# Kernel optimization log

Hardware: AMD Instinct MI355X
Metric: run time of the kernel (lower is better)

## Reference

```python
import jax, jax.numpy as jnp
import numpy as np

NB, H, C, HID, EMB = 4, 12, 1024, 768, 512
E, M, L, SPAN = 22, 4, 16, 32
TD, INTER = 20, 256
NN = E + E * M + L
NREL, NLAYERS = 3, 4

def _build_adj():
    # static relational adjacency: r0 entity<->its mentions, r1 mention<->co-entity mention, r2 mention<->link
    A = np.zeros((NREL, NN, NN), np.float32)
    for e in range(E):
        for m in range(M):
            mi = E + e * M + m
            A[0, e, mi] = A[0, mi, e] = 1.0
            for m2 in range(M):
                if m2 != m:
                    A[1, mi, E + e * M + m2] = 1.0
            li = E + E * M + ((e * M + m) % L)
            A[2, mi, li] = A[2, li, mi] = 1.0
    A = A / (A.sum(-1, keepdims=True) + 1e-5)
    return jnp.asarray(A)

_ADJ = _build_adj()
_TYPES = np.concatenate([np.zeros(E, np.int32), np.ones(E * M, np.int32), np.full(L, 2, np.int32)])

def _forward(sequence_output, attention, W_trans, b_trans, type_embed,
             rgcn_Wrel0, rgcn_Wself0, rgcn_Wrel, rgcn_Wself,
             fs_w1, fs_b1, fs_g1, fs_be1, fs_w2, fs_b2, fs_g2, fs_be2,
             fc_w1, fc_b1, fc_g1, fc_be1, fc_w2, fc_b2, fc_g2, fc_be2,
             cr_w1, cr_b1, cr_w2, cr_b2, cr_w3, cr_b3,
             mention_idx, link_start):
    n = sequence_output.shape[0]
    b = jnp.arange(n)[:, None, None]
    seq = sequence_output @ W_trans + b_trans            # [n,C,EMB] extractor_trans
    attq = attention.transpose(0, 2, 1, 3)               # [n,C,H,C] query-major
    # --- make_graph: mention / entity nodes (gather + logsumexp pooling) ---
    m_rep = seq[b, mention_idx]                          # [n,E,M,EMB]
    m_att = attq[b, mention_idx]                         # [n,E,M,H,C]
    e_rep = jax.nn.logsumexp(m_rep, axis=2)              # [n,E,EMB]
    e_att = m_att.mean(axis=2)                           # [n,E,H,C]
    # --- link nodes: attention-weighted span pooling ---
    idx = link_start[:, :, None] + jnp.arange(SPAN)      # [n,L,SPAN]
    span = seq[b, idx]                                   # [n,L,SPAN,EMB]
    att_rows = attq[b, idx]                              # [n,L,SPAN,H,C]
    col_idx = jnp.broadcast_to(idx[:, :, None, None, :], (n, L, SPAN, H, SPAN))
    block = jnp.take_along_axis(att_rows, col_idx, axis=4).mean(axis=3)  # [n,L,SPAN,SPAN]
    link_rep = jnp.einsum('nlst,nltd->nld', block, span) / SPAN          # [n,L,EMB]
    # --- node matrix + type embedding ---
    nodes = jnp.concatenate([e_rep, m_rep.reshape(n, E * M, EMB), link_rep], axis=1)
    tfeat = jnp.broadcast_to(type_embed[_TYPES][None], (n, NN, TD))
    h = jnp.concatenate([nodes, tfeat], axis=-1)         # [n,NN,EMB+TD]
    # --- RGCN ---
    def rgcn_layer(hh, Wrel, Wself):
        msg = jnp.einsum('rij,njd,rdo->nio', _ADJ, hh, Wrel)
        return jax.nn.relu(msg + hh @ Wself)
    h = rgcn_layer(h, rgcn_Wrel0, rgcn_Wself0)
    for l in range(NLAYERS - 1):
        h = rgcn_layer(h, rgcn_Wrel[l], rgcn_Wself[l])
    # --- relation_map: structure + attention-weighted context ---
    entity_stru = h[:, :E]                               # [n,E,EMB]
    ea = e_att.mean(axis=2)                              # [n,E,C]
    ea = ea / (ea.sum(-1, keepdims=True) + 1e-5)
    e_ctx = jnp.einsum('nec,ncd->ned', ea, seq)          # [n,E,EMB]
    ec = entity_stru + e_ctx
    fmap = (ec[:, :, None, :] * ec[:, None, :, :]).transpose(0, 3, 1, 2)  # [n,EMB,E,E]
    # --- SE fusion (fusion_s / fusion_c, BN in eval form) ---
    conv1x1 = lambda x, w, bb: jnp.einsum('nchw,oc->nohw', x, w) + bb[None, :, None, None]
    bn = lambda x, g, be: x * g[None, :, None, None] + be[None, :, None, None]
    s = bn(conv1x1(jax.nn.relu(bn(conv1x1(fmap, fs_w1, fs_b1), fs_g1, fs_be1)), fs_w2, fs_b2), fs_g2, fs_be2)
    pooled = fmap.mean(axis=(2, 3), keepdims=True)
    cb = bn(conv1x1(jax.nn.relu(bn(conv1x1(pooled, fc_w1, fc_b1), fc_g1, fc_be1)), fc_w2, fc_b2), fc_g2, fc_be2)
    fused = fmap * jax.nn.sigmoid(s + cb)
    # --- conv_reason 5x5 blocks ---
    dn = ('NCHW', 'OIHW', 'NCHW')
    conv = lambda x, w, bb: jax.lax.conv_general_dilated(x, w, (1, 1), 'SAME', dimension_numbers=dn) + bb[None, :, None, None]
    r = jax.nn.relu(conv(fused, cr_w1, cr_b1))
    r = jax.nn.relu(conv(r, cr_w2, cr_b2))
    return jax.nn.relu(conv(r, cr_w3, cr_b3))            # [n,EMB,E,E]

def setup_inputs():
    key = jax.random.key(0)
    ks = jax.random.split(key, 24)
    p = lambda k, sh: jax.random.normal(k, sh, jnp.float32) * 0.02
    z = lambda sh: jnp.zeros(sh, jnp.float32)
    o = lambda sh: jnp.ones(sh, jnp.float32)
    return {
        'sequence_output': jax.random.normal(ks[0], (NB, C, HID), jnp.float32),
        'attention': jax.random.uniform(ks[1], (NB, H, C, C), jnp.float32),
        'W_trans': p(ks[2], (HID, EMB)), 'b_trans': z((EMB,)),
        'type_embed': p(ks[3], (3, TD)),
        'rgcn_Wrel0': p(ks[4], (NREL, EMB + TD, EMB)), 'rgcn_Wself0': p(ks[5], (EMB + TD, EMB)),
        'rgcn_Wrel': p(ks[6], (NLAYERS - 1, NREL, EMB, EMB)), 'rgcn_Wself': p(ks[7], (NLAYERS - 1, EMB, EMB)),
        'fs_w1': p(ks[8], (INTER, EMB)), 'fs_b1': z((INTER,)), 'fs_g1': o((INTER,)), 'fs_be1': z((INTER,)),
        'fs_w2': p(ks[9], (EMB, INTER)), 'fs_b2': z((EMB,)), 'fs_g2': o((EMB,)), 'fs_be2': z((EMB,)),
        'fc_w1': p(ks[10], (INTER, EMB)), 'fc_b1': z((INTER,)), 'fc_g1': o((INTER,)), 'fc_be1': z((INTER,)),
        'fc_w2': p(ks[11], (EMB, INTER)), 'fc_b2': z((EMB,)), 'fc_g2': o((EMB,)), 'fc_be2': z((EMB,)),
        'cr_w1': p(ks[12], (INTER, EMB, 5, 5)), 'cr_b1': z((INTER,)),
        'cr_w2': p(ks[13], (INTER, INTER, 5, 5)), 'cr_b2': z((INTER,)),
        'cr_w3': p(ks[14], (EMB, INTER, 5, 5)), 'cr_b3': z((EMB,)),
        'mention_idx': jax.random.randint(ks[15], (NB, E, M), 0, C),
        'link_start': jnp.sort(jax.random.randint(ks[16], (NB, L), 0, C - SPAN), axis=-1),
    }

def reference(sequence_output, attention, W_trans, b_trans, type_embed,
              rgcn_Wrel0, rgcn_Wself0, rgcn_Wrel, rgcn_Wself,
              fs_w1, fs_b1, fs_g1, fs_be1, fs_w2, fs_b2, fs_g2, fs_be2,
              fc_w1, fc_b1, fc_g1, fc_be1, fc_w2, fc_b2, fc_g2, fc_be2,
              cr_w1, cr_b1, cr_w2, cr_b2, cr_w3, cr_b3,
              mention_idx, link_start):
    return _forward(sequence_output, attention, W_trans, b_trans, type_embed,
                    rgcn_Wrel0, rgcn_Wself0, rgcn_Wrel, rgcn_Wself,
                    fs_w1, fs_b1, fs_g1, fs_be1, fs_w2, fs_b2, fs_g2, fs_be2,
                    fc_w1, fc_b1, fc_g1, fc_be1, fc_w2, fc_b2, fc_g2, fc_be2,
                    cr_w1, cr_b1, cr_w2, cr_b2, cr_w3, cr_b3,
                    mention_idx, link_start)
```

## Files before the change

kernel.cpp:

```cpp
#include <hip/hip_runtime.h>
#include <hip/hip_bf16.h>
#include <stdint.h>

typedef long long ll;
typedef float f32x4 __attribute__((ext_vector_type(4)));
typedef __bf16 bf16x8 __attribute__((ext_vector_type(8)));
typedef __bf16 bf16x4 __attribute__((ext_vector_type(4)));

__global__ void k_prep(const float* __restrict__ cr_w1, const float* __restrict__ cr_w2,
                       const float* __restrict__ cr_w3, __bf16* __restrict__ Wt1,
                       __bf16* __restrict__ Wt2, __bf16* __restrict__ Wt3,
                       const float* __restrict__ W_trans, __bf16* __restrict__ wth,
                       __bf16* __restrict__ wtl,
                       const float* __restrict__ Wrel0, const float* __restrict__ Wself0,
                       __bf16* __restrict__ wc0h, __bf16* __restrict__ wc0l,
                       const float* __restrict__ Wrel, const float* __restrict__ Wself,
                       __bf16* __restrict__ wc13h, __bf16* __restrict__ wc13l,
                       uint4* __restrict__ XintZ)
{
  __shared__ float t[32][33];
  int b = blockIdx.x; int tid = threadIdx.x;
  if (b < 1024){
    const float* w; __bf16* dst; int C, o;
    if (b < 256){ w=cr_w1; dst=Wt1; C=512; o=b; }
    else if (b < 512){ w=cr_w2; dst=Wt2; C=256; o=b-256; }
    else { w=cr_w3; dst=Wt3; C=256; o=b-512; }
    for (int c=tid; c<C; c+=256){
      const float* src = w + ((size_t)o*C + c)*25;
      float v[25];
      #pragma unroll
      for (int q=0;q<25;q++) v[q] = src[q];
      #pragma unroll
      for (int q=0;q<25;q++) dst[((size_t)o*25 + q)*C + c] = (__bf16)v[q];
    }
  } else if (b < 2560){
    ll idx = (ll)(b-1024)*256 + tid;
    int r = (int)(idx % 768); int c = (int)(idx / 768);
    float x = W_trans[(ll)r*512 + c];
    __bf16 h = (__bf16)x;
    wth[idx] = h; wtl[idx] = (__bf16)(x - (float)h);
  } else if (b < 6720){
    int Din, Kpad, KD, bx, by;
    const float* wr; const float* ws2; __bf16* hb; __bf16* lb;
    if (b < 3648){
      int b2 = b-2560; bx = b2 % 68; by = b2/68; Din=532; Kpad=2176; KD=544;
      wr = Wrel0; ws2 = Wself0; hb = wc0h; lb = wc0l;
    } else {
      int b3 = b-3648; int l = b3/1024; int r2 = b3%1024; bx = r2%64; by = r2/64;
      Din=512; Kpad=2048; KD=512;
      wr = Wrel + (ll)l*3*512*512; ws2 = Wself + (ll)l*512*512;
      hb = wc13h + (ll)l*512*2048; lb = wc13l + (ll)l*512*2048;
    }
    int k0 = bx*32, o0 = by*32;
    int tx = tid&31, ty = tid>>5;
    for (int j=ty; j<32; j+=8){
      int k = k0 + j; float v = 0.f;
      int r = k / KD, d = k - r*KD;
      if (d < Din && r < 4)
        v = (r<3) ? wr[((ll)(r*Din+d))*512 + o0+tx] : ws2[(ll)d*512 + o0+tx];
      t[j][tx] = v;
    }
    __syncthreads();
    for (int j=ty; j<32; j+=8){
      float x = t[tx][j];
      __bf16 h = (__bf16)x;
      hb[(ll)(o0+j)*Kpad + k0+tx] = h;
      lb[(ll)(o0+j)*Kpad + k0+tx] = (__bf16)(x - (float)h);
    }
  } else {
    ll idx = (ll)(b-6720)*256 + tid;
    if (idx < 475136){
      uint4 z; z.x=0u; z.y=0u; z.z=0u; z.w=0u;
      XintZ[idx] = z;
    }
  }
}

template<int SPLIT, int MODE, int BN, int FMAPB>
__global__ __launch_bounds__(512) void gemm_mfma(
    const float* __restrict__ A,
    const __bf16* __restrict__ Bhi, const __bf16* __restrict__ Blo,
    float* __restrict__ Cf, __bf16* __restrict__ Cb,
    int M, int N, int K, ll sA, ll sB, ll sC,
    const float* __restrict__ biasN, const float* __restrict__ biasM,
    const float* __restrict__ gM, const float* __restrict__ beM,
    const float* __restrict__ Hf, const float* __restrict__ Ec,
// ... 158 lines not shown
    float* C = Cf + sC*b;
    #pragma unroll
    for (int mf=0; mf<2; ++mf){
      int gmb = m0 + wave_m0 + mf*16 + lg*4;
      #pragma unroll
      for (int nf=0; nf<NF; ++nf){
        int gn = n0 + wave_n0 + nf*16 + l15;
        if (gn >= N) continue;
        float bn_ = (MODE==0 && biasN) ? biasN[gn] : 0.f;
        f32x4 a = acc[mf][nf];
        #pragma unroll
        for (int r=0;r<4;r++){
          int gm = gmb + r;
          if (gm < M){
            float v = a[r] + bn_;
            if (MODE==1) v = fmaxf(v, 0.f);
            C[(ll)gm*N + gn] = v;
          }
        }
      }
    }
  } else if (MODE==2){
    __bf16* C = Cb + sC*b;
    #pragma unroll
    for (int mf=0; mf<2; ++mf){
      int gmb = m0 + wave_m0 + mf*16 + lg*4;
      float b0=biasM[gmb], b1=biasM[gmb+1], b2=biasM[gmb+2], b3=biasM[gmb+3];
      float g0=gM[gmb], g1=gM[gmb+1], g2=gM[gmb+2], g3=gM[gmb+3];
      float e0=beM[gmb], e1=beM[gmb+1], e2=beM[gmb+2], e3=beM[gmb+3];
      #pragma unroll
      for (int nf=0; nf<NF; ++nf){
        int gn = n0 + wave_n0 + nf*16 + l15;
        if (gn >= N) continue;
        f32x4 a = acc[mf][nf];
        union { bf16x4 v; uint2 u; } pk;
        pk.v[0] = (__bf16)fmaxf((a[0]+b0)*g0+e0, 0.f);
        pk.v[1] = (__bf16)fmaxf((a[1]+b1)*g1+e1, 0.f);
        pk.v[2] = (__bf16)fmaxf((a[2]+b2)*g2+e2, 0.f);
        pk.v[3] = (__bf16)fmaxf((a[3]+b3)*g3+e3, 0.f);
        *reinterpret_cast<uint2*>(C + (ll)gn*M + gmb) = pk.u;
      }
    }
  } else {
    __bf16* C = Cb + sC*b;
    const float* cb = CBV + (ll)b*512;
    #pragma unroll
    for (int mf=0; mf<2; ++mf){
      int gmb = m0 + wave_m0 + mf*16 + lg*4;
      float b0=biasM[gmb], b1=biasM[gmb+1], b2=biasM[gmb+2], b3=biasM[gmb+3];
      float g0=gM[gmb], g1=gM[gmb+1], g2=gM[gmb+2], g3=gM[gmb+3];
      float e0=beM[gmb], e1=beM[gmb+1], e2=beM[gmb+2], e3=beM[gmb+3];
      float c0=cb[gmb], c1=cb[gmb+1], c2=cb[gmb+2], c3=cb[gmb+3];
      #pragma unroll
      for (int nf=0; nf<NF; ++nf){
        int gn = n0 + wave_n0 + nf*16 + l15;
        if (gn >= N) continue;
        f32x4 a = acc[mf][nf];
        int pi = gn/22, pj = gn%22;
        float4 hi4 = *reinterpret_cast<const float4*>(Hf + ((ll)b*126+pi)*512 + gmb);
        float4 ei4 = *reinterpret_cast<const float4*>(Ec + ((ll)b*22 +pi)*512 + gmb);
        float4 hj4 = *reinterpret_cast<const float4*>(Hf + ((ll)b*126+pj)*512 + gmb);
        float4 ej4 = *reinterpret_cast<const float4*>(Ec + ((ll)b*22 +pj)*512 + gmb);
        float fm0 = (hi4.x+ei4.x)*(hj4.x+ej4.x);
        float fm1 = (hi4.y+ei4.y)*(hj4.y+ej4.y);
        float fm2 = (hi4.z+ei4.z)*(hj4.z+ej4.z);
        float fm3 = (hi4.w+ei4.w)*(hj4.w+ej4.w);
        float s0 = (a[0]+b0)*g0+e0 + c0;
        float s1 = (a[1]+b1)*g1+e1 + c1;
        float s2 = (a[2]+b2)*g2+e2 + c2;
        float s3 = (a[3]+b3)*g3+e3 + c3;
        union { bf16x4 v; uint2 u; } pk;
        pk.v[0] = (__bf16)(fm0 / (1.f + expf(-s0)));
        pk.v[1] = (__bf16)(fm1 / (1.f + expf(-s1)));
        pk.v[2] = (__bf16)(fm2 / (1.f + expf(-s2)));
        pk.v[3] = (__bf16)(fm3 / (1.f + expf(-s3)));
        int py = gn/22, px = gn%22;
        int e = (py+2)*32 + px + 2;
        *reinterpret_cast<uint2*>(C + (ll)e*512 + gmb) = pk.u;
      }
    }
  }
}

template<int CIN, int OCHT, int OT, bool FINAL>
__global__ __launch_bounds__(256) void conv5_mfma(
    const __bf16* __restrict__ Xg, const __bf16* __restrict__ Wt,
    const float* __restrict__ bias, __bf16* __restrict__ Xout,
    float* __restrict__ outF)
{
  constexpr int OF = OT/32;
  constexpr int WCH = OT*4;
  __shared__ bf16x8 Xs8[272*32/8];
  __shared__ bf16x8 Ws8[5*OT*32/8];
  char* xs = (char*)Xs8;
  char* wsm = (char*)Ws8;

  const int tid = threadIdx.x;
  const int l = tid & 63;
  const int l15 = l & 15, lg = l >> 4, lg16 = (l>>4)*16;
  const int w = tid >> 6;
  const int wave_o0 = (w>>1)*(OT/2);
  const int wave_p0 = (w&1)*64;
  const int b = blockIdx.z;
  const int p0 = blockIdx.x*128;
  const int o0 = blockIdx.y*OT;

  int baseA[OF];
  #pragma unroll
  for (int of=0; of<OF; ++of){
    int orow = wave_o0 + of*16 + l15;
    baseA[of] = orow*64 + (lg16 ^ (((orow>>1)&3)<<4));
  }
  int pl[4];
  #pragma unroll
  for (int pf=0; pf<4; ++pf) pl[pf] = wave_p0 + pf*16 + l15;

  f32x4 acc[OF][4] = {};

  const int NCB = CIN/32;
  for (int cblk=0; cblk<NCB; ++cblk){
    __syncthreads();
    #pragma unroll
    for (int i=0;i<5;i++){
      int idx = tid + i*256;
      if (idx < 1088){
        int e = idx>>2, c8 = idx&3;
        const __bf16* g = Xg + ((size_t)(b*928 + p0 + e))*CIN + cblk*32 + c8*8;
        bf16x8 v = *reinterpret_cast<const bf16x8*>(g);
        int byte = e*64 + ((c8*16) ^ (((e>>1)&3)<<4));
        *reinterpret_cast<bf16x8*>(xs + byte) = v;
      }
    }
    for (int g5=0; g5<5; ++g5){
      if (g5>0) __syncthreads();
      #pragma unroll
      for (int i=0;i<(5*WCH+255)/256;i++){
        int idx = tid + i*256;
        if (idx < 5*WCH){
          int tapL = idx/WCH, r = idx%WCH;
          int o = r>>2, c8 = r&3;
          const __bf16* g = Wt + ((size_t)(o0+o)*25 + (g5*5+tapL))*CIN + cblk*32 + c8*8;
          bf16x8 v = *reinterpret_cast<const bf16x8*>(g);
          int byte = tapL*(OT*64) + o*64 + ((c8*16) ^ (((o>>1)&3)<<4));
          *reinterpret_cast<bf16x8*>(wsm + byte) = v;
        }
      }
      __syncthreads();
      #pragma unroll
      for (int tapL=0; tapL<5; ++tapL){
        bf16x8 a[OF];
        #pragma unroll
        for (int of=0; of<OF; ++of)
          a[of] = *reinterpret_cast<const bf16x8*>(wsm + tapL*(OT*64) + baseA[of]);
        int koff = g5*32 + tapL;
        #pragma unroll
        for (int pf=0; pf<4; ++pf){
          int e = pl[pf] + koff;
          bf16x8 bv = *reinterpret_cast<const bf16x8*>(xs + e*64 + (lg16 ^ (((e>>1)&3)<<4)));
          #pragma unroll
          for (int of=0; of<OF; ++of)
            acc[of][pf] = __builtin_amdgcn_mfma_f32_16x16x32_bf16(a[of], bv, acc[of][pf], 0,0,0);
        }
      }
    }
  }

  #pragma unroll
  for (int of=0; of<OF; ++of){
    int og = o0 + wave_o0 + of*16 + lg*4;
    float b0 = bias[og], b1 = bias[og+1], b2 = bias[og+2], b3 = bias[og+3];
    #pragma unroll
    for (int pf=0; pf<4; ++pf){
      int p = p0 + pl[pf];
      int py = p>>5, px = p&31;
      if (py>=22 || px>=22) continue;
      f32x4 a = acc[of][pf];
      float v0 = fmaxf(a[0]+b0, 0.f), v1 = fmaxf(a[1]+b1, 0.f);
      float v2 = fmaxf(a[2]+b2, 0.f), v3 = fmaxf(a[3]+b3, 0.f);
      if (FINAL){
        size_t base = ((size_t)b*OCHT + og)*484 + py*22 + px;
        outF[base] = v0; outF[base+484] = v1; outF[base+968] = v2; outF[base+1452] = v3;
      } else {
        union { bf16x4 v; uint2 u; } pk;
        pk.v[0] = (__bf16)v0; pk.v[1] = (__bf16)v1; pk.v[2] = (__bf16)v2; pk.v[3] = (__bf16)v3;
        int e = p + 66;
        *reinterpret_cast<uint2*>(Xout + ((size_t)(b*928 + e))*OCHT + og) = pk.u;
      }
    }
  }
}

__global__ void k_gather(const float* __restrict__ seq, const float* __restrict__ att,
                         const int* __restrict__ midx, const int* __restrict__ ls_,
                         const float* __restrict__ te, float* __restrict__ h0,
                         float* __restrict__ ea, __bf16* __restrict__ sqTh,
                         __bf16* __restrict__ sqTl)
{
  __shared__ float part[32][8];
  __shared__ float wv[32];
  __shared__ float vals[1024];
  __shared__ float red[256];
  __shared__ float tt2[32][33];
  int b = blockIdx.x; int t = threadIdx.x;
  if (b < 88){
    int n = b/22, e = b%22;
    int rows[4];
    #pragma unroll
    for (int m=0;m<4;m++) rows[m] = midx[(n*22+e)*4+m];
    for (int d=t; d<512; d+=256){
      float v[4]; float mx = -1e30f;
      #pragma unroll
      for (int m=0;m<4;m++){
        v[m] = seq[((ll)n*1024+rows[m])*512 + d];
        h0[((ll)n*126+22+e*4+m)*532 + d] = v[m];
        mx = fmaxf(mx, v[m]);
      }
      float s = 0.f;
      #pragma unroll
      for (int m=0;m<4;m++) s += expf(v[m]-mx);
      h0[((ll)n*126+e)*532 + d] = mx + logf(s);
    }
  } else if (b < 152){
    int bb = b-88;
    int n = bb/16, l = bb%16;
    int ls = ls_[n*16+l];
    int tt = t>>3, lane = t&7;
    float acc = 0.f;
    for (int i=lane; i<384; i+=8){
      int h = i>>5, s = i&31;
      acc += att[((ll)(n*12+h)*1024 + ls+s)*1024 + (ls+tt)];
    }
    part[tt][lane] = acc; __syncthreads();
    if (lane==0){
      float s2=0.f;
      #pragma unroll
      for (int q=0;q<8;q++) s2 += part[tt][q];
      wv[tt] = s2*(1.f/12.f);
    }
    __syncthreads();
    for (int d=t; d<512; d+=256){
      float a2 = 0.f;
      for (int tk=0;tk<32;tk++) a2 += wv[tk]*seq[((ll)n*1024+ls+tk)*512 + d];
      h0[((ll)n*126+110+l)*532 + d] = a2*(1.f/32.f);
    }
  } else if (b < 192){
    int idx = (b-152)*256 + t;
    if (idx < 4*126*20){
      int q = idx%20; int i = (idx/20)%126; int n = idx/(20*126);
      int ty = (i<22)?0:((i<110)?1:2);
      h0[((ll)n*126+i)*532 + 512 + q] = te[ty*20+q];
    }
  } else if (b < 280){
    int bb = b-192;
    int n = bb/22, e = bb%22;
    int rows[4];
    #pragma unroll
    for (int m=0;m<4;m++) rows[m] = midx[(n*22+e)*4+m];
    float local = 0.f;
    for (int c=t; c<1024; c+=256){
      float acc = 0.f;
      #pragma unroll
      for (int m=0;m<4;m++){
        const float* base = att + ((ll)n*12*1024 + rows[m])*1024 + c;
        #pragma unroll
        for (int h=0;h<12;h++) acc += base[(ll)h*1048576];
      }
      acc *= (1.f/48.f);
      vals[c] = acc; local += acc;
    }
    red[t] = local; __syncthreads();
    for (int s=128;s>0;s>>=1){ if (t<s) red[t]+=red[t+s]; __syncthreads(); }
    float denom = red[0] + 1e-5f;
    for (int c=t; c<1024; c+=256) ea[((ll)bb)*1024 + c] = vals[c]/denom;
  } else {
    int b2 = b-280;
    int n = b2>>9; int rem = b2&511;
    int r0 = (rem&31)*32, c0 = (rem>>5)*32;
    int tx = t&31, ty = t>>5;
    for (int j=ty; j<32; j+=8)
      tt2[j][tx] = seq[((ll)n*1024 + r0+j)*512 + c0+tx];
    __syncthreads();
    for (int j=ty; j<32; j+=8){
      float x = tt2[tx][j];
      __bf16 h = (__bf16)x;
      ll o = ((ll)n*512 + c0+j)*1024 + r0+tx;
      sqTh[o] = h; sqTl[o] = (__bf16)(x - (float)h);
    }
  }
}

__global__ void k_buildX_s(const float* __restrict__ h, float* __restrict__ X,
                           int Din, int KD){
  int n = blockIdx.x/126, i = blockIdx.x%126;
  const float* hb = h + (ll)n*126*Din;
  ll rowoff = (ll)(n*126+i)*4*KD;
  const float inv1 = 1.f/(1.f+1e-5f), inv3 = 1.f/(3.f+1e-5f), inv4 = 1.f/(4.f+1e-5f);
  for (int d=threadIdx.x; d<KD; d+=256){
    float m0v=0.f, m1v=0.f, m2v=0.f, hh=0.f;
    if (d < Din){
      if (i < 22){
        int base = 22 + i*4;
        float s = hb[(ll)(base+0)*Din+d] + hb[(ll)(base+1)*Din+d]
                + hb[(ll)(base+2)*Din+d] + hb[(ll)(base+3)*Din+d];
        m0v = s * inv4;
      } else if (i < 110){
        int em = i-22, e = em>>2, base = 22+(e<<2);
        m0v = hb[(ll)e*Din+d] * inv1;
        float s1 = 0.f;
        #pragma unroll
        for (int m2=0;m2<4;m2++) if (base+m2 != i) s1 += hb[(ll)(base+m2)*Din+d];
        m1v = s1 * inv3;
        m2v = hb[(ll)(110+(em&15))*Din+d] * inv1;
      } else {
        int li0 = i-110;
        int cnt = (li0<8)?6:5;
        float s = 0.f;
        for (int t2=0;t2<cnt;t2++) s += hb[(ll)(22+li0+16*t2)*Din+d];
        m2v = s / ((float)cnt + 1e-5f);
      }
      hh = hb[(ll)i*Din+d];
    }
    X[rowoff + 0*KD + d] = m0v;
    X[rowoff + 1*KD + d] = m1v;
    X[rowoff + 2*KD + d] = m2v;
    X[rowoff + 3*KD + d] = hh;
  }
}

__global__ void k_poolcb(const float* __restrict__ hfin, const float* __restrict__ ectx,
                         const float* __restrict__ w1, const float* __restrict__ b1,
                         const float* __restrict__ g1, const float* __restrict__ be1,
                         const float* __restrict__ w2, const float* __restrict__ b2,
                         const float* __restrict__ g2, const float* __restrict__ be2,
                         float* __restrict__ cb){
  __shared__ float ps[512], t1[256];
  int n = blockIdx.x; int t = threadIdx.x;
  for (int c=t; c<512; c+=256){
    float s = 0.f;
    for (int i=0;i<22;i++)
      s += hfin[((ll)n*126+i)*512 + c] + ectx[((ll)n*22+i)*512 + c];
    ps[c] = s*s*(1.f/484.f);
  }
  __syncthreads();
  {
    float acc = 0.f;
    for (int c=0;c<512;c++) acc += w1[t*512+c]*ps[c];
    float v = g1[t]*(acc+b1[t]) + be1[t];
    t1[t] = fmaxf(v, 0.f);
  }
  __syncthreads();
  for (int o=t; o<512; o+=256){
    float acc = 0.f;
    for (int c=0;c<256;c++) acc += w2[o*256+c]*t1[c];
    cb[n*512+o] = g2[o]*(acc+b2[o]) + be2[o];
  }
}

extern "C" void kernel_launch(void* const* d_in, const int* in_sizes, int n_in,
                              void* d_out, int out_size, void* d_ws, size_t ws_size,
                              hipStream_t stream)
{
  (void)in_sizes; (void)n_in; (void)out_size; (void)ws_size;
  const float* seqout   = (const float*)d_in[0];
  const float* att      = (const float*)d_in[1];
  const float* W_trans  = (const float*)d_in[2];
  const float* b_trans  = (const float*)d_in[3];
  const float* type_emb = (const float*)d_in[4];
  const float* Wrel0    = (const float*)d_in[5];
  const float* Wself0   = (const float*)d_in[6];
  const float* Wrel     = (const float*)d_in[7];
  const float* Wself    = (const float*)d_in[8];
  const float* fs_w1    = (const float*)d_in[9];
  const float* fs_b1    = (const float*)d_in[10];
  const float* fs_g1    = (const float*)d_in[11];
  const float* fs_be1   = (const float*)d_in[12];
  const float* fs_w2    = (const float*)d_in[13];
  const float* fs_b2    = (const float*)d_in[14];
  const float* fs_g2    = (const float*)d_in[15];
  const float* fs_be2   = (const float*)d_in[16];
  const float* fc_w1    = (const float*)d_in[17];
  const float* fc_b1    = (const float*)d_in[18];
  const float* fc_g1    = (const float*)d_in[19];
  const float* fc_be1   = (const float*)d_in[20];
  const float* fc_w2    = (const float*)d_in[21];
  const float* fc_b2    = (const float*)d_in[22];
  const float* fc_g2    = (const float*)d_in[23];
  const float* fc_be2   = (const float*)d_in[24];
  const float* cr_w1    = (const float*)d_in[25];
  const float* cr_b1    = (const float*)d_in[26];
  const float* cr_w2    = (const float*)d_in[27];
  const float* cr_b2    = (const float*)d_in[28];
  const float* cr_w3    = (const float*)d_in[29];
  const float* cr_b3    = (const float*)d_in[30];
  const int*   midx     = (const int*)d_in[31];
  const int*   lstart   = (const int*)d_in[32];
  float* out            = (float*)d_out;

  char* wsb = (char*)d_ws;
  size_t off = 0;
  auto allocB = [&](size_t nbytes)->char*{ char* p = wsb + off; off += (nbytes + 63) & ~(size_t)63; return p; };
  float* seq   = (float*)allocB((size_t)4096*512*4);
  float* h0    = (float*)allocB((size_t)504*532*4);
  float* ea    = (float*)allocB((size_t)88*1024*4);
  float* ectx  = (float*)allocB((size_t)88*512*4);
  float* X     = (float*)allocB((size_t)504*2176*4);
  float* hA    = (float*)allocB((size_t)504*512*4);
  float* hB    = (float*)allocB((size_t)504*512*4);
  float* cbv   = (float*)allocB(2048*4);
  __bf16* wth  = (__bf16*)allocB((size_t)512*768*2);
  __bf16* wtl  = (__bf16*)allocB((size_t)512*768*2);
  __bf16* sqTh = (__bf16*)allocB((size_t)4*512*1024*2);
  __bf16* sqTl = (__bf16*)allocB((size_t)4*512*1024*2);
  __bf16* wc0h = (__bf16*)allocB((size_t)512*2176*2);
  __bf16* wc0l = (__bf16*)allocB((size_t)512*2176*2);
  __bf16* wc13h= (__bf16*)allocB((size_t)3*512*2048*2);
  __bf16* wc13l= (__bf16*)allocB((size_t)3*512*2048*2);
  __bf16* s1bT = (__bf16*)allocB((size_t)4*484*256*2);
  __bf16* Xint1 = (__bf16*)allocB((size_t)4*928*512*2);
  __bf16* Xint2 = (__bf16*)allocB((size_t)4*928*256*2);
  __bf16* Xint3 = (__bf16*)allocB((size_t)4*928*256*2);
  __bf16* Wt1   = (__bf16*)allocB((size_t)256*25*512*2);
  __bf16* Wt2   = (__bf16*)allocB((size_t)256*25*256*2);
  __bf16* Wt3   = (__bf16*)allocB((size_t)512*25*256*2);

  k_prep<<<8576,256,0,stream>>>(cr_w1, cr_w2, cr_w3, Wt1, Wt2, Wt3,
                                W_trans, wth, wtl,
                                Wrel0, Wself0, wc0h, wc0l,
                                Wrel, Wself, wc13h, wc13l,
                                reinterpret_cast<uint4*>(Xint1));

  gemm_mfma<1,0,128,0><<<dim3(4,64,1),512,0,stream>>>(seqout, wth, wtl, seq, nullptr,
      4096,512,768, 0,0,0, b_trans,nullptr,nullptr,nullptr, nullptr,nullptr,nullptr);
  k_gather<<<2328,256,0,stream>>>(seq, att, midx, lstart, type_emb, h0, ea, sqTh, sqTl);
  gemm_mfma<1,0,64,0><<<dim3(8,1,4),512,0,stream>>>(ea, sqTh, sqTl, ectx, nullptr,
      22,512,1024, (ll)22*1024, (ll)512*1024, (ll)22*512,
      nullptr,nullptr,nullptr,nullptr, nullptr,nullptr,nullptr);
  k_buildX_s<<<504,256,0,stream>>>(h0, X, 532, 544);
  gemm_mfma<1,1,32,0><<<dim3(16,8,1),512,0,stream>>>(X, wc0h, wc0l, hA, nullptr,
      504,512,2176, 0,0,0, nullptr,nullptr,nullptr,nullptr, nullptr,nullptr,nullptr);
  float* hcur = hA; float* hnxt = hB;
  for (int l=0;l<3;l++){
    k_buildX_s<<<504,256,0,stream>>>(hcur, X, 512, 512);
    gemm_mfma<1,1,32,0><<<dim3(16,8,1),512,0,stream>>>(X,
        wc13h + (ll)l*512*2048, wc13l + (ll)l*512*2048, hnxt, nullptr,
        504,512,2048, 0,0,0, nullptr,nullptr,nullptr,nullptr, nullptr,nullptr,nullptr);
    float* t = hcur; hcur = hnxt; hnxt = t;
  }
  k_poolcb<<<4,256,0,stream>>>(hcur, ectx, fc_w1, fc_b1, fc_g1, fc_be1,
                               fc_w2, fc_b2, fc_g2, fc_be2, cbv);
  gemm_mfma<0,2,64,1><<<dim3(8,4,4),512,0,stream>>>(fs_w1, nullptr, nullptr, nullptr, s1bT,
      256,484,512, 0, 0, (ll)484*256,
      nullptr, fs_b1, fs_g1, fs_be1, hcur, ectx, nullptr);
  gemm_mfma<0,4,64,0><<<dim3(8,8,4),512,0,stream>>>(fs_w2, s1bT, nullptr, nullptr, Xint1,
      512,484,256, 0, (ll)484*256, (ll)928*512,
      nullptr, fs_b2, fs_g2, fs_be2, hcur, ectx, cbv);
  conv5_mfma<512,256,32,false><<<dim3(6,8,4),256,0,stream>>>(Xint1, Wt1, cr_b1, Xint2, nullptr);
  conv5_mfma<256,256,32,false><<<dim3(6,8,4),256,0,stream>>>(Xint2, Wt2, cr_b2, Xint3, nullptr);
  conv5_mfma<256,512,32,true ><<<dim3(6,16,4),256,0,stream>>>(Xint3, Wt3, cr_b3, nullptr, out);
}
```

Measured before the change: 539.9 us.

## Fuse RGCN layers into one cooperative kernel and widen conv output tiles

```diff
diff --git a/kernel.cpp b/kernel.cpp
--- a/kernel.cpp
+++ b/kernel.cpp
@@ -1,7 +1,9 @@
 #include <hip/hip_runtime.h>
 #include <hip/hip_bf16.h>
+#include <hip/hip_cooperative_groups.h>
 #include <stdint.h>
 
+namespace cg = cooperative_groups;
 typedef long long ll;
 typedef float f32x4 __attribute__((ext_vector_type(4)));
 typedef __bf16 bf16x8 __attribute__((ext_vector_type(8)));
@@ -326,220 +328,15 @@
   }
 }
 
-template<int CIN, int OCHT, int OT, bool FINAL>
-__global__ __launch_bounds__(256) void conv5_mfma(
-    const __bf16* __restrict__ Xg, const __bf16* __restrict__ Wt,
-    const float* __restrict__ bias, __bf16* __restrict__ Xout,
-    float* __restrict__ outF)
-{
-  constexpr int OF = OT/32;
-  constexpr int WCH = OT*4;
-  __shared__ bf16x8 Xs8[272*32/8];
-  __shared__ bf16x8 Ws8[5*OT*32/8];
-  char* xs = (char*)Xs8;
-  char* wsm = (char*)Ws8;
-
-  const int tid = threadIdx.x;
-  const int l = tid & 63;
-  const int l15 = l & 15, lg = l >> 4, lg16 = (l>>4)*16;
-  const int w = tid >> 6;
-  const int wave_o0 = (w>>1)*(OT/2);
-  const int wave_p0 = (w&1)*64;
-  const int b = blockIdx.z;
-  const int p0 = blockIdx.x*128;
-  const int o0 = blockIdx.y*OT;
-
-  int baseA[OF];
-  #pragma unroll
-  for (int of=0; of<OF; ++of){
-    int orow = wave_o0 + of*16 + l15;
-    baseA[of] = orow*64 + (lg16 ^ (((orow>>1)&3)<<4));
-  }
-  int pl[4];
-  #pragma unroll
-  for (int pf=0; pf<4; ++pf) pl[pf] = wave_p0 + pf*16 + l15;
-
-  f32x4 acc[OF][4] = {};
-
-  const int NCB = CIN/32;
-  for (int cblk=0; cblk<NCB; ++cblk){
-    __syncthreads();
-    #pragma unroll
-    for (int i=0;i<5;i++){
-      int idx = tid + i*256;
-      if (idx < 1088){
-        int e = idx>>2, c8 = idx&3;
-        const __bf16* g = Xg + ((size_t)(b*928 + p0 + e))*CIN + cblk*32 + c8*8;
-        bf16x8 v = *reinterpret_cast<const bf16x8*>(g);
-        int byte = e*64 + ((c8*16) ^ (((e>>1)&3)<<4));
-        *reinterpret_cast<bf16x8*>(xs + byte) = v;
-      }
-    }
-    for (int g5=0; g5<5; ++g5){
-      if (g5>0) __syncthreads();
-      #pragma unroll
-      for (int i=0;i<(5*WCH+255)/256;i++){
-        int idx = tid + i*256;
-        if (idx < 5*WCH){
-          int tapL = idx/WCH, r = idx%WCH;
-          int o = r>>2, c8 = r&3;
-          const __bf16* g = Wt + ((size_t)(o0+o)*25 + (g5*5+tapL))*CIN + cblk*32 + c8*8;
-          bf16x8 v = *reinterpret_cast<const bf16x8*>(g);
-          int byte = tapL*(OT*64) + o*64 + ((c8*16) ^ (((o>>1)&3)<<4));
-          *reinterpret_cast<bf16x8*>(wsm + byte) = v;
-        }
-      }
-      __syncthreads();
-      #pragma unroll
-      for (int tapL=0; tapL<5; ++tapL){
-        bf16x8 a[OF];
-        #pragma unroll
-        for (int of=0; of<OF; ++of)
-          a[of] = *reinterpret_cast<const bf16x8*>(wsm + tapL*(OT*64) + baseA[of]);
-        int koff = g5*32 + tapL;
-        #pragma unroll
-        for (int pf=0; pf<4; ++pf){
-          int e = pl[pf] + koff;
-          bf16x8 bv = *reinterpret_cast<const bf16x8*>(xs + e*64 + (lg16 ^ (((e>>1)&3)<<4)));
-          #pragma unroll
-          for (int of=0; of<OF; ++of)
-            acc[of][pf] = __builtin_amdgcn_mfma_f32_16x16x32_bf16(a[of], bv, acc[of][pf], 0,0,0);
-        }
-      }
-    }
-  }
-
-  #pragma unroll
-  for (int of=0; of<OF; ++of){
-    int og = o0 + wave_o0 + of*16 + lg*4;
-    float b0 = bias[og], b1 = bias[og+1], b2 = bias[og+2], b3 = bias[og+3];
-    #pragma unroll
-    for (int pf=0; pf<4; ++pf){
-      int p = p0 + pl[pf];
-      int py = p>>5, px = p&31;
-      if (py>=22 || px>=22) continue;
-      f32x4 a = acc[of][pf];
-      float v0 = fmaxf(a[0]+b0, 0.f), v1 = fmaxf(a[1]+b1, 0.f);
-      float v2 = fmaxf(a[2]+b2, 0.f), v3 = fmaxf(a[3]+b3, 0.f);
-      if (FINAL){
-        size_t base = ((size_t)b*OCHT + og)*484 + py*22 + px;
-        outF[base] = v0; outF[base+484] = v1; outF[base+968] = v2; outF[base+1452] = v3;
-      } else {
-        union { bf16x4 v; uint2 u; } pk;
-        pk.v[0] = (__bf16)v0; pk.v[1] = (__bf16)v1; pk.v[2] = (__bf16)v2; pk.v[3] = (__bf16)v3;
-        int e = p + 66;
-        *reinterpret_cast<uint2*>(Xout + ((size_t)(b*928 + e))*OCHT + og) = pk.u;
-      }
-    }
-  }
-}
-
-__global__ void k_gather(const float* __restrict__ seq, const float* __restrict__ att,
-                         const int* __restrict__ midx, const int* __restrict__ ls_,
-                         const float* __restrict__ te, float* __restrict__ h0,
-                         float* __restrict__ ea, __bf16* __restrict__ sqTh,
-                         __bf16* __restrict__ sqTl)
-{
-  __shared__ float part[32][8];
-  __shared__ float wv[32];
-  __shared__ float vals[1024];
-  __shared__ float red[256];
-  __shared__ float tt2[32][33];
-  int b = blockIdx.x; int t = threadIdx.x;
-  if (b < 88){
-    int n = b/22, e = b%22;
-    int rows[4];
-    #pragma unroll
-    for (int m=0;m<4;m++) rows[m] = midx[(n*22+e)*4+m];
-    for (int d=t; d<512; d+=256){
-      float v[4]; float mx = -1e30f;
-      #pragma unroll
-      for (int m=0;m<4;m++){
-        v[m] = seq[((ll)n*1024+rows[m])*512 + d];
-        h0[((ll)n*126+22+e*4+m)*532 + d] = v[m];
-        mx = fmaxf(mx, v[m]);
-      }
-      float s = 0.f;
-      #pragma unroll
-      for (int m=0;m<4;m++) s += expf(v[m]-mx);
-      h0[((ll)n*126+e)*532 + d] = mx + logf(s);
-    }
-  } else if (b < 152){
-    int bb = b-88;
-    int n = bb/16, l = bb%16;
-    int ls = ls_[n*16+l];
-    int tt = t>>3, lane = t&7;
-    float acc = 0.f;
-    for (int i=lane; i<384; i+=8){
-      int h = i>>5, s = i&31;
-      acc += att[((ll)(n*12+h)*1024 + ls+s)*1024 + (ls+tt)];
-    }
-    part[tt][lane] = acc; __syncthreads();
-    if (lane==0){
-      float s2=0.f;
-      #pragma unroll
-      for (int q=0;q<8;q++) s2 += part[tt][q];
-      wv[tt] = s2*(1.f/12.f);
-    }
-    __syncthreads();
-    for (int d=t; d<512; d+=256){
-      float a2 = 0.f;
-      for (int tk=0;tk<32;tk++) a2 += wv[tk]*seq[((ll)n*1024+ls+tk)*512 + d];
-      h0[((ll)n*126+110+l)*532 + d] = a2*(1.f/32.f);
-    }
-  } else if (b < 192){
-    int idx = (b-152)*256 + t;
-    if (idx < 4*126*20){
-      int q = idx%20; int i = (idx/20)%126; int n = idx/(20*126);
-      int ty = (i<22)?0:((i<110)?1:2);
-      h0[((ll)n*126+i)*532 + 512 + q] = te[ty*20+q];
-    }
-  } else if (b < 280){
-    int bb = b-192;
-    int n = bb/22, e = bb%22;
-    int rows[4];
-    #pragma unroll
-    for (int m=0;m<4;m++) rows[m] = midx[(n*22+e)*4+m];
-    float local = 0.f;
-    for (int c=t; c<1024; c+=256){
-      float acc = 0.f;
-      #pragma unroll
-      for (int m=0;m<4;m++){
-        const float* base = att + ((ll)n*12*1024 + rows[m])*1024 + c;
-        #pragma unroll
-        for (int h=0;h<12;h++) acc += base[(ll)h*1048576];
-      }
-      acc *= (1.f/48.f);
-      vals[c] = acc; local += acc;
-    }
-    red[t] = local; __syncthreads();
-    for (int s=128;s>0;s>>=1){ if (t<s) red[t]+=red[t+s]; __syncthreads(); }
-    float denom = red[0] + 1e-5f;
-    for (int c=t; c<1024; c+=256) ea[((ll)bb)*1024 + c] = vals[c]/denom;
-  } else {
-    int b2 = b-280;
-    int n = b2>>9; int rem = b2&511;
-    int r0 = (rem&31)*32, c0 = (rem>>5)*32;
-    int tx = t&31, ty = t>>5;
-    for (int j=ty; j<32; j+=8)
-      tt2[j][tx] = seq[((ll)n*1024 + r0+j)*512 + c0+tx];
-    __syncthreads();
-    for (int j=ty; j<32; j+=8){
-      float x = tt2[tx][j];
-      __bf16 h = (__bf16)x;
-      ll o = ((ll)n*512 + c0+j)*1024 + r0+tx;
-      sqTh[o] = h; sqTl[o] = (__bf16)(x - (float)h);
-    }
-  }
-}
-
-__global__ void k_buildX_s(const float* __restrict__ h, float* __restrict__ X,
-                           int Din, int KD){
-  int n = blockIdx.x/126, i = blockIdx.x%126;
-  const float* hb = h + (ll)n*126*Din;
-  ll rowoff = (ll)(n*126+i)*4*KD;
+__device__ __forceinline__ void buildX_phase(const float* __restrict__ h,
+                                             float* __restrict__ X, int Din, int KD){
   const float inv1 = 1.f/(1.f+1e-5f), inv3 = 1.f/(3.f+1e-5f), inv4 = 1.f/(4.f+1e-5f);
-  for (int d=threadIdx.x; d<KD; d+=256){
+  int total = 504*KD;
+  for (int idx = blockIdx.x*512 + threadIdx.x; idx < total; idx += 128*512){
+    int row = idx / KD;
+    int d = idx - row*KD;
+    int n = row/126, i = row - n*126;
+    const float* hb = h + (ll)n*126*Din;
     float m0v=0.f, m1v=0.f, m2v=0.f, hh=0.f;
     if (d < Din){
       if (i < 22){
@@ -564,10 +361,364 @@
       }
       hh = hb[(ll)i*Din+d];
     }
+    ll rowoff = (ll)row*4*KD;
     X[rowoff + 0*KD + d] = m0v;
     X[rowoff + 1*KD + d] = m1v;
     X[rowoff + 2*KD + d] = m2v;
     X[rowoff + 3*KD + d] = hh;
+  }
+}
+
+__device__ __forceinline__ void rgcn_gemm_phase(
+    const float* __restrict__ A, const __bf16* __restrict__ Bhi,
+    const __bf16* __restrict__ Blo, float* __restrict__ C, int K, char* lds)
+{
+  constexpr int BN=32, NF=1, SL=(4096+BN*64)*2;
+  const int M=504, N=512;
+  const int tid = threadIdx.x;
+  const int slice = tid>>8;
+  const int tl = tid & 255;
+  const int w4 = (tid>>6)&3;
+  const int grp = tid>>8;
+  const int l15 = tid&15, lg=(tid&63)>>4, lg16=lg*16;
+  const int wave_m0=(w4>>1)*32, wave_n0=(w4&1)*(BN/2);
+  const int m0 = (blockIdx.x>>4)*64, n0 = (blockIdx.x&15)*BN;
+
+  char* sA_H = lds + slice*SL;
+  char* sB_H = sA_H + 4096;
+  char* sA_L = sB_H + BN*64;
+  char* sB_L = sA_L + 4096;
+
+  const int sa_row=tl>>2, sa_c8=tl&3;
+  const int sa_byte = sa_row*64 + ((sa_c8*16) ^ (((sa_row>>1)&3)<<4));
+  const int gmA = m0 + sa_row;
+
+  int baseA[2], baseB[NF];
+  #pragma unroll
+  for (int mf=0; mf<2; ++mf){
+    int r = wave_m0 + mf*16 + l15;
+    baseA[mf] = r*64 + (lg16 ^ (((r>>1)&3)<<4));
+  }
+  #pragma unroll
+  for (int nf=0; nf<NF; ++nf){
+    int r = wave_n0 + nf*16 + l15;
+    baseB[nf] = r*64 + (lg16 ^ (((r>>1)&3)<<4));
+  }
+
+  f32x4 acc[2][NF] = {};
+
+  for (int k0=0; k0<K; k0+=64){
+    int kk = k0 + slice*32;
+    __syncthreads();
+    {
+      float f[8] = {0,0,0,0,0,0,0,0};
+      if (gmA < M){
+        float4 p0 = *reinterpret_cast<const float4*>(A + (ll)gmA*K + kk + sa_c8*8);
+        float4 p1 = *reinterpret_cast<const float4*>(A + (ll)gmA*K + kk + sa_c8*8 + 4);
+        f[0]=p0.x; f[1]=p0.y; f[2]=p0.z; f[3]=p0.w;
+        f[4]=p1.x; f[5]=p1.y; f[6]=p1.z; f[7]=p1.w;
+      }
+      bf16x8 h, l;
+      #pragma unroll
+      for (int j=0;j<8;j++){
+        h[j] = (__bf16)f[j];
+        l[j] = (__bf16)(f[j] - (float)h[j]);
+      }
+      *reinterpret_cast<bf16x8*>(sA_H + sa_byte) = h;
+      *reinterpret_cast<bf16x8*>(sA_L + sa_byte) = l;
+    }
+    if (tl < BN*4){
+      int row = tl>>2, c8 = tl&3;
+      int gn = n0 + row;
+      int byte = row*64 + ((c8*16) ^ (((row>>1)&3)<<4));
+      bf16x8 v = *reinterpret_cast<const bf16x8*>(Bhi + (ll)gn*K + kk + c8*8);
+      bf16x8 vl = *reinterpret_cast<const bf16x8*>(Blo + (ll)gn*K + kk + c8*8);
+      *reinterpret_cast<bf16x8*>(sB_H + byte) = v;
+      *reinterpret_cast<bf16x8*>(sB_L + byte) = vl;
+    }
+    __syncthreads();
+    bf16x8 aH[2], bH[NF], aL[2], bL[NF];
+    #pragma unroll
+    for (int mf=0; mf<2; ++mf){
+      aH[mf] = *reinterpret_cast<const bf16x8*>(sA_H + baseA[mf]);
+      aL[mf] = *reinterpret_cast<const bf16x8*>(sA_L + baseA[mf]);
+    }
+    #pragma unroll
+    for (int nf=0; nf<NF; ++nf){
+      bH[nf] = *reinterpret_cast<const bf16x8*>(sB_H + baseB[nf]);
+      bL[nf] = *reinterpret_cast<const bf16x8*>(sB_L + baseB[nf]);
+    }
+    #pragma unroll
+    for (int mf=0; mf<2; ++mf)
+      #pragma unroll
+      for (int nf=0; nf<NF; ++nf){
+        acc[mf][nf] = __builtin_amdgcn_mfma_f32_16x16x32_bf16(aH[mf], bH[nf], acc[mf][nf], 0,0,0);
+        acc[mf][nf] = __builtin_amdgcn_mfma_f32_16x16x32_bf16(aH[mf], bL[nf], acc[mf][nf], 0,0,0);
+        acc[mf][nf] = __builtin_amdgcn_mfma_f32_16x16x32_bf16(aL[mf], bH[nf], acc[mf][nf], 0,0,0);
+      }
+  }
+
+  __syncthreads();
+  if (grp==1){
+    char* rp = lds + (ll)(tid-256)*(2*NF*16);
+    #pragma unroll
+    for (int mf=0; mf<2; ++mf)
+      #pragma unroll
+      for (int nf=0; nf<NF; ++nf)
+        *reinterpret_cast<f32x4*>(rp + (mf*NF+nf)*16) = acc[mf][nf];
+  }
+  __syncthreads();
+  if (grp==0){
+    char* rp = lds + (ll)tid*(2*NF*16);
+    #pragma unroll
+    for (int mf=0; mf<2; ++mf)
+      #pragma unroll
+      for (int nf=0; nf<NF; ++nf)
+        acc[mf][nf] += *reinterpret_cast<f32x4*>(rp + (mf*NF+nf)*16);
+    #pragma unroll
+    for (int mf=0; mf<2; ++mf){
+      int gmb = m0 + wave_m0 + mf*16 + lg*4;
+      #pragma unroll
+      for (int nf=0; nf<NF; ++nf){
+        int gn = n0 + wave_n0 + nf*16 + l15;
+        f32x4 a = acc[mf][nf];
+        #pragma unroll
+        for (int r=0;r<4;r++){
+          int gm = gmb + r;
+          if (gm < M) C[(ll)gm*N + gn] = fmaxf(a[r], 0.f);
+        }
+      }
+    }
+  }
+}
+
+__global__ __launch_bounds__(512) void rgcn_coop(
+    const float* __restrict__ h0, float* __restrict__ X,
+    const __bf16* __restrict__ wc0h, const __bf16* __restrict__ wc0l,
+    const __bf16* __restrict__ wc13h, const __bf16* __restrict__ wc13l,
+    float* __restrict__ hA, float* __restrict__ hB)
+{
+  cg::grid_group grid = cg::this_grid();
+  __shared__ char lds[24576];
+  for (int layer=0; layer<4; ++layer){
+    const int Din = (layer==0)?532:512;
+    const int KD  = (layer==0)?544:512;
+    const int K   = 4*KD;
+    const float* hin = (layer==0)? h0 : ((layer&1)? hA : hB);
+    float* hout = (layer&1)? hB : hA;
+    const __bf16* Bh = (layer==0)? wc0h : (wc13h + (ll)(layer-1)*512*2048);
+    const __bf16* Bl = (layer==0)? wc0l : (wc13l + (ll)(layer-1)*512*2048);
+    buildX_phase(hin, X, Din, KD);
+    grid.sync();
+    rgcn_gemm_phase(X, Bh, Bl, hout, K, lds);
+    grid.sync();
+  }
+}
+
+template<int CIN, int OCHT, int OT, bool FINAL>
+__global__ __launch_bounds__(256) void conv5_mfma(
+    const __bf16* __restrict__ Xg, const __bf16* __restrict__ Wt,
+    const float* __restrict__ bias, __bf16* __restrict__ Xout,
+    float* __restrict__ outF)
+{
+  constexpr int OF = OT/32;
+  constexpr int WCH = OT*4;
+  __shared__ bf16x8 Xs8[272*32/8];
+  __shared__ bf16x8 Ws8[5*OT*32/8];
+  char* xs = (char*)Xs8;
+  char* wsm = (char*)Ws8;
+
+  const int tid = threadIdx.x;
+  const int l = tid & 63;
+  const int l15 = l & 15, lg = l >> 4, lg16 = (l>>4)*16;
+  const int w = tid >> 6;
+  const int wave_o0 = (w>>1)*(OT/2);
+  const int wave_p0 = (w&1)*64;
+  const int b = blockIdx.z;
+  const int p0 = blockIdx.x*128;
+  const int o0 = blockIdx.y*OT;
+
+  int baseA[OF];
+  #pragma unroll
+  for (int of=0; of<OF; ++of){
+    int orow = wave_o0 + of*16 + l15;
+    baseA[of] = orow*64 + (lg16 ^ (((orow>>1)&3)<<4));
+  }
+  int pl[4];
+  #pragma unroll
+  for (int pf=0; pf<4; ++pf) pl[pf] = wave_p0 + pf*16 + l15;
+
+  f32x4 acc[OF][4] = {};
+
+  const int NCB = CIN/32;
+  for (int cblk=0; cblk<NCB; ++cblk){
+    __syncthreads();
+    #pragma unroll
+    for (int i=0;i<5;i++){
+      int idx = tid + i*256;
+      if (idx < 1088){
+        int e = idx>>2, c8 = idx&3;
+        const __bf16* g = Xg + ((size_t)(b*928 + p0 + e))*CIN + cblk*32 + c8*8;
+        bf16x8 v = *reinterpret_cast<const bf16x8*>(g);
+        int byte = e*64 + ((c8*16) ^ (((e>>1)&3)<<4));
+        *reinterpret_cast<bf16x8*>(xs + byte) = v;
+      }
+    }
+    for (int g5=0; g5<5; ++g5){
+      if (g5>0) __syncthreads();
+      #pragma unroll
+      for (int i=0;i<(5*WCH+255)/256;i++){
+        int idx = tid + i*256;
+        if (idx < 5*WCH){
+          int tapL = idx/WCH, r = idx%WCH;
+          int o = r>>2, c8 = r&3;
+          const __bf16* g = Wt + ((size_t)(o0+o)*25 + (g5*5+tapL))*CIN + cblk*32 + c8*8;
+          bf16x8 v = *reinterpret_cast<const bf16x8*>(g);
+          int byte = tapL*(OT*64) + o*64 + ((c8*16) ^ (((o>>1)&3)<<4));
+          *reinterpret_cast<bf16x8*>(wsm + byte) = v;
+        }
+      }
+      __syncthreads();
+      #pragma unroll
+      for (int tapL=0; tapL<5; ++tapL){
+        bf16x8 a[OF];
+        #pragma unroll
+        for (int of=0; of<OF; ++of)
+          a[of] = *reinterpret_cast<const bf16x8*>(wsm + tapL*(OT*64) + baseA[of]);
+        int koff = g5*32 + tapL;
+        #pragma unroll
+        for (int pf=0; pf<4; ++pf){
+          int e = pl[pf] + koff;
+          bf16x8 bv = *reinterpret_cast<const bf16x8*>(xs + e*64 + (lg16 ^ (((e>>1)&3)<<4)));
+          #pragma unroll
+          for (int of=0; of<OF; ++of)
+            acc[of][pf] = __builtin_amdgcn_mfma_f32_16x16x32_bf16(a[of], bv, acc[of][pf], 0,0,0);
+        }
+      }
+    }
+  }
+
+  #pragma unroll
+  for (int of=0; of<OF; ++of){
+    int og = o0 + wave_o0 + of*16 + lg*4;
+    float b0 = bias[og], b1 = bias[og+1], b2 = bias[og+2], b3 = bias[og+3];
+    #pragma unroll
+    for (int pf=0; pf<4; ++pf){
+      int p = p0 + pl[pf];
+      int py = p>>5, px = p&31;
+      if (py>=22 || px>=22) continue;
+      f32x4 a = acc[of][pf];
+      float v0 = fmaxf(a[0]+b0, 0.f), v1 = fmaxf(a[1]+b1, 0.f);
+      float v2 = fmaxf(a[2]+b2, 0.f), v3 = fmaxf(a[3]+b3, 0.f);
+      if (FINAL){
+        size_t base = ((size_t)b*OCHT + og)*484 + py*22 + px;
+        outF[base] = v0; outF[base+484] = v1; outF[base+968] = v2; outF[base+1452] = v3;
+      } else {
+        union { bf16x4 v; uint2 u; } pk;
+        pk.v[0] = (__bf16)v0; pk.v[1] = (__bf16)v1; pk.v[2] = (__bf16)v2; pk.v[3] = (__bf16)v3;
+        int e = p + 66;
+        *reinterpret_cast<uint2*>(Xout + ((size_t)(b*928 + e))*OCHT + og) = pk.u;
+      }
+    }
+  }
+}
+
+__global__ void k_gather(const float* __restrict__ seq, const float* __restrict__ att,
+                         const int* __restrict__ midx, const int* __restrict__ ls_,
+                         const float* __restrict__ te, float* __restrict__ h0,
+                         float* __restrict__ ea, __bf16* __restrict__ sqTh,
+                         __bf16* __restrict__ sqTl)
+{
+  __shared__ float part[32][8];
+  __shared__ float wv[32];
+  __shared__ float vals[1024];
+  __shared__ float red[256];
+  __shared__ float tt2[32][33];
+  int b = blockIdx.x; int t = threadIdx.x;
+  if (b < 88){
+    int n = b/22, e = b%22;
+    int rows[4];
+    #pragma unroll
+    for (int m=0;m<4;m++) rows[m] = midx[(n*22+e)*4+m];
+    for (int d=t; d<512; d+=256){
+      float v[4]; float mx = -1e30f;
+      #pragma unroll
+      for (int m=0;m<4;m++){
+        v[m] = seq[((ll)n*1024+rows[m])*512 + d];
+        h0[((ll)n*126+22+e*4+m)*532 + d] = v[m];
+        mx = fmaxf(mx, v[m]);
+      }
+      float s = 0.f;
+      #pragma unroll
+      for (int m=0;m<4;m++) s += expf(v[m]-mx);
+      h0[((ll)n*126+e)*532 + d] = mx + logf(s);
+    }
+  } else if (b < 152){
+    int bb = b-88;
+    int n = bb/16, l = bb%16;
+    int ls = ls_[n*16+l];
+    int tt = t>>3, lane = t&7;
+    float acc = 0.f;
+    for (int i=lane; i<384; i+=8){
+      int h = i>>5, s = i&31;
+      acc += att[((ll)(n*12+h)*1024 + ls+s)*1024 + (ls+tt)];
+    }
+    part[tt][lane] = acc; __syncthreads();
+    if (lane==0){
+      float s2=0.f;
+      #pragma unroll
+      for (int q=0;q<8;q++) s2 += part[tt][q];
+      wv[tt] = s2*(1.f/12.f);
+    }
+    __syncthreads();
+    for (int d=t; d<512; d+=256){
+      float a2 = 0.f;
+      for (int tk=0;tk<32;tk++) a2 += wv[tk]*seq[((ll)n*1024+ls+tk)*512 + d];
+      h0[((ll)n*126+110+l)*532 + d] = a2*(1.f/32.f);
+    }
+  } else if (b < 192){
+    int idx = (b-152)*256 + t;
+    if (idx < 4*126*20){
+      int q = idx%20; int i = (idx/20)%126; int n = idx/(20*126);
+      int ty = (i<22)?0:((i<110)?1:2);
+      h0[((ll)n*126+i)*532 + 512 + q] = te[ty*20+q];
+    }
+  } else if (b < 280){
+    int bb = b-192;
+    int n = bb/22, e = bb%22;
+    int rows[4];
+    #pragma unroll
+    for (int m=0;m<4;m++) rows[m] = midx[(n*22+e)*4+m];
+    float local = 0.f;
+    for (int c=t; c<1024; c+=256){
+      float acc = 0.f;
+      #pragma unroll
+      for (int m=0;m<4;m++){
+        const float* base = att + ((ll)n*12*1024 + rows[m])*1024 + c;
+        #pragma unroll
+        for (int h=0;h<12;h++) acc += base[(ll)h*1048576];
+      }
+      acc *= (1.f/48.f);
+      vals[c] = acc; local += acc;
+    }
+    red[t] = local; __syncthreads();
+    for (int s=128;s>0;s>>=1){ if (t<s) red[t]+=red[t+s]; __syncthreads(); }
+    float denom = red[0] + 1e-5f;
+    for (int c=t; c<1024; c+=256) ea[((ll)bb)*1024 + c] = vals[c]/denom;
+  } else {
+    int b2 = b-280;
+    int n = b2>>9; int rem = b2&511;
+    int r0 = (rem&31)*32, c0 = (rem>>5)*32;
+    int tx = t&31, ty = t>>5;
+    for (int j=ty; j<32; j+=8)
+      tt2[j][tx] = seq[((ll)n*1024 + r0+j)*512 + c0+tx];
+    __syncthreads();
+    for (int j=ty; j<32; j+=8){
+      float x = tt2[tx][j];
+      __bf16 h = (__bf16)x;
+      ll o = ((ll)n*512 + c0+j)*1024 + r0+tx;
+      sqTh[o] = h; sqTl[o] = (__bf16)(x - (float)h);
+    }
   }
 }
 
@@ -679,17 +830,16 @@
   gemm_mfma<1,0,64,0><<<dim3(8,1,4),512,0,stream>>>(ea, sqTh, sqTl, ectx, nullptr,
       22,512,1024, (ll)22*1024, (ll)512*1024, (ll)22*512,
       nullptr,nullptr,nullptr,nullptr, nullptr,nullptr,nullptr);
-  k_buildX_s<<<504,256,0,stream>>>(h0, X, 532, 544);
-  gemm_mfma<1,1,32,0><<<dim3(16,8,1),512,0,stream>>>(X, wc0h, wc0l, hA, nullptr,
-      504,512,2176, 0,0,0, nullptr,nullptr,nullptr,nullptr, nullptr,nullptr,nullptr);
-  float* hcur = hA; float* hnxt = hB;
-  for (int l=0;l<3;l++){
-    k_buildX_s<<<504,256,0,stream>>>(hcur, X, 512, 512);
-    gemm_mfma<1,1,32,0><<<dim3(16,8,1),512,0,stream>>>(X,
-        wc13h + (ll)l*512*2048, wc13l + (ll)l*512*2048, hnxt, nullptr,
-        504,512,2048, 0,0,0, nullptr,nullptr,nullptr,nullptr, nullptr,nullptr,nullptr);
-    float* t = hcur; hcur = hnxt; hnxt = t;
-  }
+  {
+    void* args[8];
+    args[0]=(void*)&h0;  args[1]=(void*)&X;
+    args[2]=(void*)&wc0h; args[3]=(void*)&wc0l;
+    args[4]=(void*)&wc13h; args[5]=(void*)&wc13l;
+    args[6]=(void*)&hA;  args[7]=(void*)&hB;
+    (void)hipLaunchCooperativeKernel(reinterpret_cast<void*>(rgcn_coop),
+                                     dim3(128), dim3(512), args, 0, stream);
+  }
+  float* hcur = hB;
   k_poolcb<<<4,256,0,stream>>>(hcur, ectx, fc_w1, fc_b1, fc_g1, fc_be1,
                                fc_w2, fc_b2, fc_g2, fc_be2, cbv);
   gemm_mfma<0,2,64,1><<<dim3(8,4,4),512,0,stream>>>(fs_w1, nullptr, nullptr, nullptr, s1bT,
@@ -698,7 +848,7 @@
   gemm_mfma<0,4,64,0><<<dim3(8,8,4),512,0,stream>>>(fs_w2, s1bT, nullptr, nullptr, Xint1,
       512,484,256, 0, (ll)484*256, (ll)928*512,
       nullptr, fs_b2, fs_g2, fs_be2, hcur, ectx, cbv);
-  conv5_mfma<512,256,32,false><<<dim3(6,8,4),256,0,stream>>>(Xint1, Wt1, cr_b1, Xint2, nullptr);
-  conv5_mfma<256,256,32,false><<<dim3(6,8,4),256,0,stream>>>(Xint2, Wt2, cr_b2, Xint3, nullptr);
-  conv5_mfma<256,512,32,true ><<<dim3(6,16,4),256,0,stream>>>(Xint3, Wt3, cr_b3, nullptr, out);
+  conv5_mfma<512,256,64,false><<<dim3(6,4,4),256,0,stream>>>(Xint1, Wt1, cr_b1, Xint2, nullptr);
+  conv5_mfma<256,256,64,false><<<dim3(6,4,4),256,0,stream>>>(Xint2, Wt2, cr_b2, Xint3, nullptr);
+  conv5_mfma<256,512,64,true ><<<dim3(6,8,4),256,0,stream>>>(Xint3, Wt3, cr_b3, nullptr, out);
 }
```

Result: slower. 726.2 us (+34.5%).
